# Kernel tuning notes

Measured on AMD Instinct MI355X. Metric: run time of the kernel, lower is better.

## Reference

```python
import jax, jax.numpy as jnp
import numpy as np

NY, NX, DIM = 4096, 50000, 3
RADIUS = 1.4
BOX = 14.3  # chosen so ~16 y-neighbors per x point at radius 1.4
LAYERS = [3, 128, 256, 3]  # kernel_in_dim=3 -> hidden [128,256] -> dim=3


def _radius_neighbors(x, y, r):
    """Brute-force radius search: edges (x_index i, nbr_index j) with |x_i - y_j| <= r."""
    r2 = r * r
    xi, yj = [], []
    for s in range(0, x.shape[0], 5000):
        xc = x[s:s + 5000]
        d2 = ((xc[:, None, :] - y[None, :, :]) ** 2).sum(-1)
        ii, jj = np.nonzero(d2 <= r2)
        xi.append(ii + s)
        yj.append(jj)
    return np.concatenate(yj).astype(np.int64), np.concatenate(xi).astype(np.int64)


def setup_inputs() -> dict:
    rng = np.random.default_rng(0)
    y = rng.uniform(0.0, BOX, (NY, DIM)).astype(np.float32)   # rom_ic points
    x = rng.uniform(0.0, BOX, (NX, DIM)).astype(np.float32)   # fom_ic points
    f_y = rng.standard_normal((NY, DIM)).astype(np.float32)   # rom_f values
    nbr_index, x_index = _radius_neighbors(x, y, RADIUS)

    key = jax.random.key(0)
    ks = jax.random.split(key, 3)
    params = {}
    for i in range(3):
        fan_in = LAYERS[i]
        params[f"W{i+1}"] = (jax.random.normal(ks[i], (LAYERS[i], LAYERS[i + 1]), jnp.float32)
                             / np.float32(np.sqrt(fan_in)))
        params[f"b{i+1}"] = jnp.zeros((LAYERS[i + 1],), jnp.float32)

    return dict(rom_ic=jnp.asarray(y)[None], fom_ic=jnp.asarray(x)[None],
                rom_f=jnp.asarray(f_y)[None],
                nbr_index=jnp.asarray(nbr_index), x_index=jnp.asarray(x_index),
                **params)


def _kernel_mlp(h, W1, b1, W2, b2, W3, b3):
    h = jax.nn.gelu(h @ W1 + b1)
    h = jax.nn.gelu(h @ W2 + b2)
    return h @ W3 + b3


def reference(rom_ic, fom_ic, rom_f, W1, b1, W2, b2, W3, b3, nbr_index, x_index):
    y = rom_ic[0]      # [NY,3] source points
    x = fom_ic[0]      # [NX,3] target points
    f_y = rom_f[0]     # [NY,3] source function values

    rel = y[nbr_index] - x[x_index]                    # [E,3] per-edge kernel input
    k = _kernel_mlp(rel, W1, b1, W2, b2, W3, b3)       # [E,3] kernel values
    msg = k * f_y[nbr_index]                           # 'linear' transform: k(x,y) * f(y)

    num = jax.ops.segment_sum(msg, x_index, num_segments=x.shape[0])        # [NX,3]
    cnt = jax.ops.segment_sum(jnp.ones((msg.shape[0],), msg.dtype), x_index,
                              num_segments=x.shape[0])                      # [NX]
    out = num / jnp.maximum(cnt, 1.0)[:, None]         # mean over neighbors (0 if none)
    return out[None]                                    # [1, NX, 3]
```

## Files before the change

kernel.cpp:

```cpp
#include <hip/hip_runtime.h>
#include <hip/hip_bf16.h>

typedef __bf16 bf16x8 __attribute__((ext_vector_type(8)));
typedef float  f32x4  __attribute__((ext_vector_type(4)));
typedef float  f32x2  __attribute__((ext_vector_type(2)));
typedef float  f32x16 __attribute__((ext_vector_type(16)));
typedef int    i32x4  __attribute__((ext_vector_type(4)));

__device__ __forceinline__ f32x2 gelu2(f32x2 x) {
    f32x2 x2 = x * x;
    f32x2 t  = x2 * 0.044715f + 1.0f;
    f32x2 a  = (x * -1.5957691216057308f) * t;
    f32x2 e  = { __expf(a.x), __expf(a.y) };
    f32x2 d  = e + 1.0f;
    f32x2 r  = { __builtin_amdgcn_rcpf(d.x), __builtin_amdgcn_rcpf(d.y) };
    return x * r;
}

__device__ __forceinline__ unsigned int pack2bf(float a, float b) {
    unsigned short ua = __builtin_bit_cast(unsigned short, (__bf16)a);
    unsigned short ub = __builtin_bit_cast(unsigned short, (__bf16)b);
    return (unsigned int)ua | ((unsigned int)ub << 16);
}

__global__ void prep_weights(const float* __restrict__ W2, const float* __restrict__ W3,
                             __bf16* __restrict__ w2t, __bf16* __restrict__ w3t) {
    int idx = blockIdx.x * 256 + threadIdx.x;
    if (idx < 128 * 256) {
        int k = idx >> 8;
        int u = idx & 255;
        w2t[u * 128 + k] = (__bf16)W2[idx];
    } else if (idx < 128 * 256 + 32 * 256) {
        int t = idx - 128 * 256;
        int d = t >> 8;
        int u = t & 255;
        w3t[t] = (__bf16)(d < 3 ? W3[u * 3 + d] : 0.0f);
    }
}

__launch_bounds__(256, 4)
__global__ void edge_mlp(const float* __restrict__ y, const float* __restrict__ x,
                         const float* __restrict__ fy,
                         const int* __restrict__ nbr, const int* __restrict__ xidx,
                         const float* __restrict__ W1, const float* __restrict__ b1,
                         const __bf16* __restrict__ w2t, const float* __restrict__ b2,
                         const __bf16* __restrict__ w3t, const float* __restrict__ b3,
                         float* __restrict__ out, int E) {
    __shared__ __attribute__((aligned(16))) __bf16 g2s[64 * 128];
    __shared__ __attribute__((aligned(16))) float rels4[64][4];
    __shared__ float fys[64][3];
    __shared__ int   is[64];
    __shared__ float b2s[256];
    __shared__ float out3w[4][64][3];
    __shared__ float msg3[64][3];

    const int tid  = threadIdx.x;
    const int base = blockIdx.x * 64;

    if (tid < 64) {
        int g = base + tid;
        if (g < E) {
            int j = nbr[g];
            int i = xidx[g];
            is[tid] = i;
            f32x4 rr = { y[j*3+0] - x[i*3+0],
                         y[j*3+1] - x[i*3+1],
                         y[j*3+2] - x[i*3+2], 0.0f };
            *(f32x4*)&rels4[tid][0] = rr;
            fys[tid][0] = fy[j*3+0];
            fys[tid][1] = fy[j*3+1];
            fys[tid][2] = fy[j*3+2];
        } else {
            is[tid] = -1;
            *(f32x4*)&rels4[tid][0] = (f32x4){0.0f, 0.0f, 0.0f, 0.0f};
            fys[tid][0] = fys[tid][1] = fys[tid][2] = 0.0f;
        }
    }
    b2s[tid] = b2[tid];
    __syncthreads();

    {
        int u  = tid & 127;
        int e0 = tid >> 7;
        float w0 = W1[u], w1 = W1[128 + u], w2 = W1[256 + u], bb = b1[u];
        #pragma unroll
        for (int r = 0; r < 32; r += 2) {
            int ea = e0 + 2 * r;
            int eb = ea + 2;
            f32x4 ra = *(const f32x4*)&rels4[ea][0];
            f32x4 rb = *(const f32x4*)&rels4[eb][0];
            float prea = fmaf(ra.x, w0, fmaf(ra.y, w1, fmaf(ra.z, w2, bb)));
            float preb = fmaf(rb.x, w0, fmaf(rb.y, w1, fmaf(rb.z, w2, bb)));
            f32x2 g = gelu2((f32x2){prea, preb});
            g2s[ea * 128 + (u ^ ((ea & 7) << 3))] = (__bf16)g.x;
            g2s[eb * 128 + (u ^ ((eb & 7) << 3))] = (__bf16)g.y;
        }
    }
    __syncthreads();

    const int w    = tid >> 6;
    const int lane = tid & 63;
    const int l31  = lane & 31;
    const int b    = lane >> 5;

    unsigned int pk[2][2][8];

    #pragma unroll
    for (int ut2 = 0; ut2 < 2; ++ut2) {
        f32x16 acc[2];
        #pragma unroll
        for (int et2 = 0; et2 < 2; ++et2)
            #pragma unroll
            for (int q = 0; q < 16; ++q)
                acc[et2][q] = 0.0f;

        #pragma unroll
        for (int kt = 0; kt < 8; ++kt) {
            int kc = kt * 16 + b * 8;
            bf16x8 bfrg[2];
            #pragma unroll
            for (int et2 = 0; et2 < 2; ++et2) {
                int row = et2 * 32 + l31;
                bfrg[et2] = *(const bf16x8*)&g2s[row * 128 + (kc ^ ((row & 7) << 3))];
            }
            int u = (2 * w + ut2) * 32 + l31;
            bf16x8 afrg = *(const bf16x8*)&w2t[u * 128 + kc];
            #pragma unroll
            for (int et2 = 0; et2 < 2; ++et2)
                acc[et2] = __builtin_amdgcn_mfma_f32_32x32x16_bf16(
                    afrg, bfrg[et2], acc[et2], 0, 0, 0);
        }

        int u0 = (2 * w + ut2) * 32 + 4 * b;
        f32x4 b2q[4];
        #pragma unroll
        for (int g = 0; g < 4; ++g)
            b2q[g] = *(const f32x4*)&b2s[u0 + 8 * g];
        #pragma unroll
        for (int et2 = 0; et2 < 2; ++et2) {
            #pragma unroll
            for (int g = 0; g < 4; ++g) {
                f32x2 s01 = { acc[et2][4*g+0] + b2q[g][0], acc[et2][4*g+1] + b2q[g][1] };
                f32x2 s23 = { acc[et2][4*g+2] + b2q[g][2], acc[et2][4*g+3] + b2q[g][3] };
                f32x2 g01 = gelu2(s01);
                f32x2 g23 = gelu2(s23);
                pk[ut2][et2][2*g+0] = pack2bf(g01.x, g01.y);
                pk[ut2][et2][2*g+1] = pack2bf(g23.x, g23.y);
            }
        }
    }

    f32x16 acc3[2];
    #pragma unroll
    for (int et2 = 0; et2 < 2; ++et2)
        #pragma unroll
        for (int q = 0; q < 16; ++q)
            acc3[et2][q] = 0.0f;

    #pragma unroll
    for (int kt = 0; kt < 4; ++kt) {
        const int ut2 = kt >> 1, ki = kt & 1;
        bf16x8 a3 = *(const bf16x8*)&w3t[l31 * 256 + w * 64 + kt * 16 + b * 8];
        #pragma unroll
        for (int et2 = 0; et2 < 2; ++et2) {
            int w0_ = (int)pk[ut2][et2][4*ki + 0];
            int w1_ = (int)pk[ut2][et2][4*ki + 1];
            int w2_ = (int)pk[ut2][et2][4*ki + 2];
            int w3_ = (int)pk[ut2][et2][4*ki + 3];
            auto p02 = __builtin_amdgcn_permlane32_swap(w0_, w2_, false, false);
            auto p13 = __builtin_amdgcn_permlane32_swap(w1_, w3_, false, false);
            i32x4 fri = { static_cast<int>(p02[0]), static_cast<int>(p13[0]),
                          static_cast<int>(p02[1]), static_cast<int>(p13[1]) };
            bf16x8 bfr = __builtin_bit_cast(bf16x8, fri);
            acc3[et2] = __builtin_amdgcn_mfma_f32_32x32x16_bf16(a3, bfr, acc3[et2], 0, 0, 0);
        }
    }

    if (b == 0) {
        #pragma unroll
        for (int et2 = 0; et2 < 2; ++et2) {
            int e = et2 * 32 + l31;
            out3w[w][e][0] = acc3[et2][0];
            out3w[w][e][1] = acc3[et2][1];
            out3w[w][e][2] = acc3[et2][2];
        }
    }
    __syncthreads();

    if (tid < 192) {
        int e = tid / 3, d = tid - 3 * (tid / 3);
        float s = out3w[0][e][d] + out3w[1][e][d] + out3w[2][e][d] + out3w[3][e][d];
        msg3[e][d] = (s + b3[d]) * fys[e][d];
    }
    __syncthreads();

    if (tid < 64) {
        int i = is[tid];
        bool leader = (i >= 0) && (tid == 0 || is[tid - 1] != i);
        if (leader) {
            float s0 = 0.0f, s1 = 0.0f, s2 = 0.0f;
            int j = tid;
            while (j < 64 && is[j] == i) {
                s0 += msg3[j][0]; s1 += msg3[j][1]; s2 += msg3[j][2]; ++j;
            }
            unsafeAtomicAdd(&out[i*3+0], s0);
            unsafeAtomicAdd(&out[i*3+1], s1);
            unsafeAtomicAdd(&out[i*3+2], s2);
        }
    }
}

__global__ void finalize_div(float* __restrict__ out, const int* __restrict__ xidx,
                             int E, int nx) {
    int i = blockIdx.x * blockDim.x + threadIdx.x;
    if (i >= nx) return;
    int lo = 0, hi = E;
    while (lo < hi) { int mid = (lo + hi) >> 1; if (xidx[mid] < i) lo = mid + 1; else hi = mid; }
    int start = lo;
    hi = E;
    while (lo < hi) { int mid = (lo + hi) >> 1; if (xidx[mid] < i + 1) lo = mid + 1; else hi = mid; }
    int cnt = lo - start;
    float inv = 1.0f / (float)(cnt > 1 ? cnt : 1);
    out[i*3+0] *= inv;
    out[i*3+1] *= inv;
    out[i*3+2] *= inv;
}

extern "C" void kernel_launch(void* const* d_in, const int* in_sizes, int n_in,
                              void* d_out, int out_size, void* d_ws, size_t ws_size,
                              hipStream_t stream) {
    const float* y   = (const float*)d_in[0];
    const float* x   = (const float*)d_in[1];
    const float* fyp = (const float*)d_in[2];
    const int*   nbr = (const int*)d_in[3];
    const int*   xix = (const int*)d_in[4];
    const float* W1  = (const float*)d_in[5];
    const float* b1  = (const float*)d_in[6];
    const float* W2  = (const float*)d_in[7];
    const float* b2  = (const float*)d_in[8];
    const float* W3  = (const float*)d_in[9];
    const float* b3  = (const float*)d_in[10];
    float* out = (float*)d_out;

    int E  = in_sizes[3];
    int nx = in_sizes[1] / 3;
    __bf16* w2t = (__bf16*)d_ws;
    __bf16* w3t = (__bf16*)((char*)d_ws + 65536);

    hipMemsetAsync(d_out, 0, (size_t)out_size * sizeof(float), stream);
    prep_weights<<<160, 256, 0, stream>>>(W2, W3, w2t, w3t);

    int ntiles = (E + 63) / 64;
    edge_mlp<<<ntiles, 256, 0, stream>>>(y, x, fyp, nbr, xix, W1, b1, w2t, b2, w3t, b3, out, E);

    finalize_div<<<(nx + 255) / 256, 256, 0, stream>>>(out, xix, E, nx);
}
```

Baseline: 158.5 us.

## Give each wave its own 32 edges and keep all MLP layers in registers

Each wave now handles 32 edges end to end, where before four waves split the hidden units of 64 shared edges. Layer 1 runs on MFMA with a padded bf16 W1, and its GELU outputs are turned into B fragments in registers through permlane32 swaps. This removes the g2s LDS staging, most block barriers, and the cross-wave reduction of layer-3 partials. In exchange, every wave streams all of W2 from global/L2, and the relative coordinates are now rounded to bf16, which can lower layer-1 accuracy.

```diff
diff --git a/kernel.cpp b/kernel.cpp
--- a/kernel.cpp
+++ b/kernel.cpp
@@ -23,18 +23,34 @@
     return (unsigned int)ua | ((unsigned int)ub << 16);
 }
 
+__device__ __forceinline__ bf16x8 frag_from_pk(unsigned int q0, unsigned int q1,
+                                               unsigned int q2, unsigned int q3) {
+    auto p02 = __builtin_amdgcn_permlane32_swap((int)q0, (int)q2, false, false);
+    auto p13 = __builtin_amdgcn_permlane32_swap((int)q1, (int)q3, false, false);
+    i32x4 fri = { static_cast<int>(p02[0]), static_cast<int>(p13[0]),
+                  static_cast<int>(p02[1]), static_cast<int>(p13[1]) };
+    return __builtin_bit_cast(bf16x8, fri);
+}
+
 __global__ void prep_weights(const float* __restrict__ W2, const float* __restrict__ W3,
-                             __bf16* __restrict__ w2t, __bf16* __restrict__ w3t) {
+                             const float* __restrict__ W1,
+                             __bf16* __restrict__ w2t, __bf16* __restrict__ w3t,
+                             __bf16* __restrict__ w1tp) {
     int idx = blockIdx.x * 256 + threadIdx.x;
-    if (idx < 128 * 256) {
+    if (idx < 32768) {
         int k = idx >> 8;
         int u = idx & 255;
         w2t[u * 128 + k] = (__bf16)W2[idx];
-    } else if (idx < 128 * 256 + 32 * 256) {
-        int t = idx - 128 * 256;
+    } else if (idx < 32768 + 8192) {
+        int t = idx - 32768;
         int d = t >> 8;
         int u = t & 255;
         w3t[t] = (__bf16)(d < 3 ? W3[u * 3 + d] : 0.0f);
+    } else if (idx < 32768 + 8192 + 2048) {
+        int t = idx - 40960;
+        int u = t >> 4;
+        int k = t & 15;
+        w1tp[t] = (k < 3) ? (__bf16)W1[k * 128 + u] : (__bf16)0.0f;
     }
 }
 
@@ -42,170 +58,142 @@
 __global__ void edge_mlp(const float* __restrict__ y, const float* __restrict__ x,
                          const float* __restrict__ fy,
                          const int* __restrict__ nbr, const int* __restrict__ xidx,
-                         const float* __restrict__ W1, const float* __restrict__ b1,
+                         const __bf16* __restrict__ w1tp, const float* __restrict__ b1,
                          const __bf16* __restrict__ w2t, const float* __restrict__ b2,
                          const __bf16* __restrict__ w3t, const float* __restrict__ b3,
                          float* __restrict__ out, int E) {
-    __shared__ __attribute__((aligned(16))) __bf16 g2s[64 * 128];
-    __shared__ __attribute__((aligned(16))) float rels4[64][4];
-    __shared__ float fys[64][3];
-    __shared__ int   is[64];
+    __shared__ __attribute__((aligned(16))) __bf16 relT[4][32][16];
+    __shared__ float b1s[128];
     __shared__ float b2s[256];
-    __shared__ float out3w[4][64][3];
-    __shared__ float msg3[64][3];
+    __shared__ float msgS[4][32][3];
+    __shared__ int   isS[4][32];
 
     const int tid  = threadIdx.x;
-    const int base = blockIdx.x * 64;
-
-    if (tid < 64) {
-        int g = base + tid;
-        if (g < E) {
-            int j = nbr[g];
-            int i = xidx[g];
-            is[tid] = i;
-            f32x4 rr = { y[j*3+0] - x[i*3+0],
-                         y[j*3+1] - x[i*3+1],
-                         y[j*3+2] - x[i*3+2], 0.0f };
-            *(f32x4*)&rels4[tid][0] = rr;
-            fys[tid][0] = fy[j*3+0];
-            fys[tid][1] = fy[j*3+1];
-            fys[tid][2] = fy[j*3+2];
-        } else {
-            is[tid] = -1;
-            *(f32x4*)&rels4[tid][0] = (f32x4){0.0f, 0.0f, 0.0f, 0.0f};
-            fys[tid][0] = fys[tid][1] = fys[tid][2] = 0.0f;
-        }
-    }
-    b2s[tid] = b2[tid];
-    __syncthreads();
-
-    {
-        int u  = tid & 127;
-        int e0 = tid >> 7;
-        float w0 = W1[u], w1 = W1[128 + u], w2 = W1[256 + u], bb = b1[u];
-        #pragma unroll
-        for (int r = 0; r < 32; r += 2) {
-            int ea = e0 + 2 * r;
-            int eb = ea + 2;
-            f32x4 ra = *(const f32x4*)&rels4[ea][0];
-            f32x4 rb = *(const f32x4*)&rels4[eb][0];
-            float prea = fmaf(ra.x, w0, fmaf(ra.y, w1, fmaf(ra.z, w2, bb)));
-            float preb = fmaf(rb.x, w0, fmaf(rb.y, w1, fmaf(rb.z, w2, bb)));
-            f32x2 g = gelu2((f32x2){prea, preb});
-            g2s[ea * 128 + (u ^ ((ea & 7) << 3))] = (__bf16)g.x;
-            g2s[eb * 128 + (u ^ ((eb & 7) << 3))] = (__bf16)g.y;
-        }
-    }
-    __syncthreads();
-
-    const int w    = tid >> 6;
+    const int wid  = tid >> 6;
     const int lane = tid & 63;
     const int l31  = lane & 31;
     const int b    = lane >> 5;
 
-    unsigned int pk[2][2][8];
+    const int g = blockIdx.x * 128 + wid * 32 + l31;
+
+    int   iidx = -1;
+    float fy0 = 0.0f, fy1 = 0.0f, fy2 = 0.0f;
+    if (b == 0) {
+        bf16x8 rv = { (__bf16)0.0f, (__bf16)0.0f, (__bf16)0.0f, (__bf16)0.0f,
+                      (__bf16)0.0f, (__bf16)0.0f, (__bf16)0.0f, (__bf16)0.0f };
+        if (g < E) {
+            int j = nbr[g];
+            iidx  = xidx[g];
+            rv[0] = (__bf16)(y[j*3+0] - x[iidx*3+0]);
+            rv[1] = (__bf16)(y[j*3+1] - x[iidx*3+1]);
+            rv[2] = (__bf16)(y[j*3+2] - x[iidx*3+2]);
+            fy0 = fy[j*3+0];
+            fy1 = fy[j*3+1];
+            fy2 = fy[j*3+2];
+        }
+        *(bf16x8*)&relT[wid][l31][0] = rv;
+        *(bf16x8*)&relT[wid][l31][8] = (bf16x8){ (__bf16)0.0f, (__bf16)0.0f, (__bf16)0.0f, (__bf16)0.0f,
+                                                 (__bf16)0.0f, (__bf16)0.0f, (__bf16)0.0f, (__bf16)0.0f };
+    }
+    b2s[tid] = b2[tid];
+    if (tid < 128) b1s[tid] = b1[tid];
+    __syncthreads();
+
+    bf16x8 relB = *(const bf16x8*)&relT[wid][l31][b * 8];
+    bf16x8 B2[8];
 
     #pragma unroll
-    for (int ut2 = 0; ut2 < 2; ++ut2) {
-        f32x16 acc[2];
-        #pragma unroll
-        for (int et2 = 0; et2 < 2; ++et2)
-            #pragma unroll
-            for (int q = 0; q < 16; ++q)
-                acc[et2][q] = 0.0f;
-
+    for (int ut1 = 0; ut1 < 4; ++ut1) {
+        f32x16 c;
+        #pragma unroll
+        for (int q = 0; q < 16; ++q) c[q] = 0.0f;
+        bf16x8 a1 = *(const bf16x8*)&w1tp[(ut1 * 32 + l31) * 16 + b * 8];
+        c = __builtin_amdgcn_mfma_f32_32x32x16_bf16(a1, relB, c, 0, 0, 0);
+
+        int u0 = ut1 * 32 + 4 * b;
+        f32x4 b1q[4];
+        #pragma unroll
+        for (int gq = 0; gq < 4; ++gq)
+            b1q[gq] = *(const f32x4*)&b1s[u0 + 8 * gq];
+
+        unsigned int pw[8];
+        #pragma unroll
+        for (int gq = 0; gq < 4; ++gq) {
+            f32x2 s01 = { c[4*gq+0] + b1q[gq][0], c[4*gq+1] + b1q[gq][1] };
+            f32x2 s23 = { c[4*gq+2] + b1q[gq][2], c[4*gq+3] + b1q[gq][3] };
+            f32x2 g01 = gelu2(s01);
+            f32x2 g23 = gelu2(s23);
+            pw[2*gq+0] = pack2bf(g01.x, g01.y);
+            pw[2*gq+1] = pack2bf(g23.x, g23.y);
+        }
+        B2[2*ut1+0] = frag_from_pk(pw[0], pw[1], pw[2], pw[3]);
+        B2[2*ut1+1] = frag_from_pk(pw[4], pw[5], pw[6], pw[7]);
+    }
+
+    f32x16 acc3;
+    #pragma unroll
+    for (int q = 0; q < 16; ++q) acc3[q] = 0.0f;
+
+    #pragma unroll
+    for (int ut = 0; ut < 8; ++ut) {
+        f32x16 c;
+        #pragma unroll
+        for (int q = 0; q < 16; ++q) c[q] = 0.0f;
         #pragma unroll
         for (int kt = 0; kt < 8; ++kt) {
-            int kc = kt * 16 + b * 8;
-            bf16x8 bfrg[2];
-            #pragma unroll
-            for (int et2 = 0; et2 < 2; ++et2) {
-                int row = et2 * 32 + l31;
-                bfrg[et2] = *(const bf16x8*)&g2s[row * 128 + (kc ^ ((row & 7) << 3))];
-            }
-            int u = (2 * w + ut2) * 32 + l31;
-            bf16x8 afrg = *(const bf16x8*)&w2t[u * 128 + kc];
-            #pragma unroll
-            for (int et2 = 0; et2 < 2; ++et2)
-                acc[et2] = __builtin_amdgcn_mfma_f32_32x32x16_bf16(
-                    afrg, bfrg[et2], acc[et2], 0, 0, 0);
-        }
-
-        int u0 = (2 * w + ut2) * 32 + 4 * b;
+            bf16x8 a2 = *(const bf16x8*)&w2t[(ut * 32 + l31) * 128 + kt * 16 + b * 8];
+            c = __builtin_amdgcn_mfma_f32_32x32x16_bf16(a2, B2[kt], c, 0, 0, 0);
+        }
+
+        int u0 = ut * 32 + 4 * b;
         f32x4 b2q[4];
         #pragma unroll
-        for (int g = 0; g < 4; ++g)
-            b2q[g] = *(const f32x4*)&b2s[u0 + 8 * g];
-        #pragma unroll
-        for (int et2 = 0; et2 < 2; ++et2) {
-            #pragma unroll
-            for (int g = 0; g < 4; ++g) {
-                f32x2 s01 = { acc[et2][4*g+0] + b2q[g][0], acc[et2][4*g+1] + b2q[g][1] };
-                f32x2 s23 = { acc[et2][4*g+2] + b2q[g][2], acc[et2][4*g+3] + b2q[g][3] };
-                f32x2 g01 = gelu2(s01);
-                f32x2 g23 = gelu2(s23);
-                pk[ut2][et2][2*g+0] = pack2bf(g01.x, g01.y);
-                pk[ut2][et2][2*g+1] = pack2bf(g23.x, g23.y);
-            }
-        }
-    }
-
-    f32x16 acc3[2];
-    #pragma unroll
-    for (int et2 = 0; et2 < 2; ++et2)
-        #pragma unroll
-        for (int q = 0; q < 16; ++q)
-            acc3[et2][q] = 0.0f;
-
-    #pragma unroll
-    for (int kt = 0; kt < 4; ++kt) {
-        const int ut2 = kt >> 1, ki = kt & 1;
-        bf16x8 a3 = *(const bf16x8*)&w3t[l31 * 256 + w * 64 + kt * 16 + b * 8];
-        #pragma unroll
-        for (int et2 = 0; et2 < 2; ++et2) {
-            int w0_ = (int)pk[ut2][et2][4*ki + 0];
-            int w1_ = (int)pk[ut2][et2][4*ki + 1];
-            int w2_ = (int)pk[ut2][et2][4*ki + 2];
-            int w3_ = (int)pk[ut2][et2][4*ki + 3];
-            auto p02 = __builtin_amdgcn_permlane32_swap(w0_, w2_, false, false);
-            auto p13 = __builtin_amdgcn_permlane32_swap(w1_, w3_, false, false);
-            i32x4 fri = { static_cast<int>(p02[0]), static_cast<int>(p13[0]),
-                          static_cast<int>(p02[1]), static_cast<int>(p13[1]) };
-            bf16x8 bfr = __builtin_bit_cast(bf16x8, fri);
-            acc3[et2] = __builtin_amdgcn_mfma_f32_32x32x16_bf16(a3, bfr, acc3[et2], 0, 0, 0);
+        for (int gq = 0; gq < 4; ++gq)
+            b2q[gq] = *(const f32x4*)&b2s[u0 + 8 * gq];
+
+        unsigned int pw[8];
+        #pragma unroll
+        for (int gq = 0; gq < 4; ++gq) {
+            f32x2 s01 = { c[4*gq+0] + b2q[gq][0], c[4*gq+1] + b2q[gq][1] };
+            f32x2 s23 = { c[4*gq+2] + b2q[gq][2], c[4*gq+3] + b2q[gq][3] };
+            f32x2 g01 = gelu2(s01);
+            f32x2 g23 = gelu2(s23);
+            pw[2*gq+0] = pack2bf(g01.x, g01.y);
+            pw[2*gq+1] = pack2bf(g23.x, g23.y);
+        }
+
+        #pragma unroll
+        for (int ki = 0; ki < 2; ++ki) {
+            bf16x8 bfr = frag_from_pk(pw[4*ki+0], pw[4*ki+1], pw[4*ki+2], pw[4*ki+3]);
+            bf16x8 a3  = *(const bf16x8*)&w3t[l31 * 256 + ut * 32 + ki * 16 + b * 8];
+            acc3 = __builtin_amdgcn_mfma_f32_32x32x16_bf16(a3, bfr, acc3, 0, 0, 0);
         }
     }
 
     if (b == 0) {
-        #pragma unroll
-        for (int et2 = 0; et2 < 2; ++et2) {
-            int e = et2 * 32 + l31;
-            out3w[w][e][0] = acc3[et2][0];
-            out3w[w][e][1] = acc3[et2][1];
-            out3w[w][e][2] = acc3[et2][2];
-        }
-    }
-    __syncthreads();
-
-    if (tid < 192) {
-        int e = tid / 3, d = tid - 3 * (tid / 3);
-        float s = out3w[0][e][d] + out3w[1][e][d] + out3w[2][e][d] + out3w[3][e][d];
-        msg3[e][d] = (s + b3[d]) * fys[e][d];
-    }
-    __syncthreads();
-
-    if (tid < 64) {
-        int i = is[tid];
-        bool leader = (i >= 0) && (tid == 0 || is[tid - 1] != i);
+        float m0 = 0.0f, m1 = 0.0f, m2 = 0.0f;
+        if (iidx >= 0) {
+            m0 = (acc3[0] + b3[0]) * fy0;
+            m1 = (acc3[1] + b3[1]) * fy1;
+            m2 = (acc3[2] + b3[2]) * fy2;
+        }
+        msgS[wid][l31][0] = m0;
+        msgS[wid][l31][1] = m1;
+        msgS[wid][l31][2] = m2;
+        isS[wid][l31] = iidx;
+        bool leader = (iidx >= 0) && (l31 == 0 || isS[wid][l31 - 1] != iidx);
         if (leader) {
             float s0 = 0.0f, s1 = 0.0f, s2 = 0.0f;
-            int j = tid;
-            while (j < 64 && is[j] == i) {
-                s0 += msg3[j][0]; s1 += msg3[j][1]; s2 += msg3[j][2]; ++j;
+            int j = l31;
+            while (j < 32 && isS[wid][j] == iidx) {
+                s0 += msgS[wid][j][0];
+                s1 += msgS[wid][j][1];
+                s2 += msgS[wid][j][2];
+                ++j;
             }
-            unsafeAtomicAdd(&out[i*3+0], s0);
-            unsafeAtomicAdd(&out[i*3+1], s1);
-            unsafeAtomicAdd(&out[i*3+2], s2);
+            unsafeAtomicAdd(&out[iidx*3+0], s0);
+            unsafeAtomicAdd(&out[iidx*3+1], s1);
+            unsafeAtomicAdd(&out[iidx*3+2], s2);
         }
     }
 }
@@ -244,14 +232,15 @@
 
     int E  = in_sizes[3];
     int nx = in_sizes[1] / 3;
-    __bf16* w2t = (__bf16*)d_ws;
-    __bf16* w3t = (__bf16*)((char*)d_ws + 65536);
+    __bf16* w2t  = (__bf16*)d_ws;
+    __bf16* w3t  = (__bf16*)((char*)d_ws + 65536);
+    __bf16* w1tp = (__bf16*)((char*)d_ws + 81920);
 
     hipMemsetAsync(d_out, 0, (size_t)out_size * sizeof(float), stream);
-    prep_weights<<<160, 256, 0, stream>>>(W2, W3, w2t, w3t);
-
-    int ntiles = (E + 63) / 64;
-    edge_mlp<<<ntiles, 256, 0, stream>>>(y, x, fyp, nbr, xix, W1, b1, w2t, b2, w3t, b3, out, E);
+    prep_weights<<<168, 256, 0, stream>>>(W2, W3, W1, w2t, w3t, w1tp);
+
+    int nblocks = (E + 127) / 128;
+    edge_mlp<<<nblocks, 256, 0, stream>>>(y, x, fyp, nbr, xix, w1tp, b1, w2t, b2, w3t, b3, out, E);
 
     finalize_div<<<(nx + 255) / 256, 256, 0, stream>>>(out, xix, E, nx);
 }
```

Result: slower. 229.9 us (+45.1%).
